# Performance work log

Hardware: AMD Instinct MI355X
Metric: run time of the kernel (lower is better)

Reference implementation:

```python
import jax, jax.numpy as jnp
import numpy as np

N_NODES = 10000
N_EDGES = 160000
LN_EPS = 1e-5
BN_EPS = 1e-5


def _leaky(x, slope=0.2):
    return jnp.where(x >= 0, x, slope * x)


def _gat_conv(x, edge_index, W, att_src, att_dst, bias, concat):
    # x: [N, Din]; W: [Din, H*C]; att_*: [H, C]
    H, C = att_src.shape
    h = (x @ W).reshape(-1, H, C)                       # [N, H, C]
    a_src = jnp.einsum('nhc,hc->nh', h, att_src)        # [N, H]
    a_dst = jnp.einsum('nhc,hc->nh', h, att_dst)
    src, dst = edge_index[0], edge_index[1]
    logits = _leaky(a_src[src] + a_dst[dst], 0.2)       # [E, H]
    # segment softmax over incoming edges of each dst node
    m = jax.ops.segment_max(logits, dst, num_segments=N_NODES)
    e = jnp.exp(logits - m[dst])
    denom = jax.ops.segment_sum(e, dst, num_segments=N_NODES)
    alpha = e / denom[dst]                              # [E, H]
    msg = h[src] * alpha[:, :, None]                    # [E, H, C]
    out = jax.ops.segment_sum(msg, dst, num_segments=N_NODES)  # [N, H, C]
    if concat:
        out = out.reshape(-1, H * C)
    else:
        out = out.mean(axis=1)
    return out + bias


def setup_inputs() -> dict:
    key = jax.random.key(0)
    ks = jax.random.split(key, 10)
    d_in, H, C = 128, 8, 64
    W = H * C  # 512
    return {
        'x': jax.random.normal(ks[0], (N_NODES, d_in), jnp.float32),
        'edge_index': jax.random.randint(ks[1], (2, N_EDGES), 0, N_NODES, jnp.int64),
        'ft_W': jax.random.normal(ks[2], (d_in, W), jnp.float32) * (1.0 / np.sqrt(d_in)),
        'ft_b': jnp.zeros((W,), jnp.float32),
        'ln_g': jnp.ones((W,), jnp.float32),
        'ln_b': jnp.zeros((W,), jnp.float32),
        'W1': jax.random.normal(ks[3], (W, H * C), jnp.float32) * (1.0 / np.sqrt(W)),
        'att_src1': jax.random.normal(ks[4], (H, C), jnp.float32) * 0.1,
        'att_dst1': jax.random.normal(ks[5], (H, C), jnp.float32) * 0.1,
        'b1': jnp.zeros((W,), jnp.float32),
        'bn_g': jnp.ones((W,), jnp.float32),
        'bn_b': jnp.zeros((W,), jnp.float32),
        'bn_mean': jnp.zeros((W,), jnp.float32),
        'bn_var': jnp.ones((W,), jnp.float32),
        'W2': jax.random.normal(ks[6], (W, H * 2), jnp.float32) * (1.0 / np.sqrt(W)),
        'att_src2': jax.random.normal(ks[7], (H, 2), jnp.float32) * 0.1,
        'att_dst2': jax.random.normal(ks[8], (H, 2), jnp.float32) * 0.1,
        'b2': jnp.zeros((2,), jnp.float32),
    }


def reference(x, edge_index, ft_W, ft_b, ln_g, ln_b, W1, att_src1, att_dst1, b1,
              bn_g, bn_b, bn_mean, bn_var, W2, att_src2, att_dst2, b2):
    # feature transform: Linear -> LayerNorm -> LeakyReLU(0.2)
    h = x @ ft_W + ft_b
    mu = h.mean(axis=-1, keepdims=True)
    var = h.var(axis=-1, keepdims=True)
    h = (h - mu) * jax.lax.rsqrt(var + LN_EPS) * ln_g + ln_b
    h = _leaky(h, 0.2)
    # GAT layer 1 (concat heads) -> BatchNorm (eval) -> ReLU  (dropout = identity in eval)
    h = _gat_conv(h, edge_index, W1, att_src1, att_dst1, b1, concat=True)
    h = (h - bn_mean) * jax.lax.rsqrt(bn_var + BN_EPS) * bn_g + bn_b
    h = jax.nn.relu(h)
    # GAT layer 2 (mean heads) -> logits [N, 2]
    logits = _gat_conv(h, edge_index, W2, att_src2, att_dst2, b2, concat=False)
    return logits
```

## Files before the change

kernel.cpp:

```cpp
#include <hip/hip_runtime.h>
#include <hip/hip_bf16.h>
#include <math.h>

#define N_NODES 10000
#define N_EDGES 160000
#define DIN 128
#define DW 512
#define NHEAD 8
#define NC 64
#define MPAD 10112
#define GEMM_BLKS 316

typedef unsigned short ushort_t;
typedef __attribute__((ext_vector_type(8))) short bf16x8;
typedef __attribute__((ext_vector_type(4))) float f32x4;

__device__ inline ushort_t f2bf(float v) {
    unsigned u = __builtin_bit_cast(unsigned, v);
    return (ushort_t)((u + 0x7fff + ((u >> 16) & 1)) >> 16);
}
__device__ inline float bf2f(ushort_t h) {
    return __builtin_bit_cast(float, (unsigned)h << 16);
}

__device__ __forceinline__ size_t swz_idx(int rb, int r, int kp, int nkt) {
    int kt = kp >> 6, kc = kp & 63;
    return ((size_t)(rb * nkt + kt)) * 8192 + r * 64 + (kc ^ ((r & 7) << 3));
}

__device__ __forceinline__ void gld16(const ushort_t* g, ushort_t* l) {
    __builtin_amdgcn_global_load_lds(
        (const __attribute__((address_space(1))) void*)g,
        (__attribute__((address_space(3))) void*)l, 16, 0, 0);
}

__global__ void k_prep(const float* __restrict__ x, const float* __restrict__ ftW,
                       const float* __restrict__ W1f,
                       ushort_t* __restrict__ Ax, ushort_t* __restrict__ Bx,
                       ushort_t* __restrict__ B1,
                       int* __restrict__ cnt, int* __restrict__ cursor) {
    int bid = blockIdx.x, t = threadIdx.x;
    if (bid < 5056) {
        int i = bid * 256 + t;
        int n = i >> 7, k = i & 127;
        float v = (n < N_NODES) ? x[n * DIN + k] : 0.f;
        ushort_t h = f2bf(v);
        ushort_t l = f2bf(v - bf2f(h));
        int rb = n >> 7, r = n & 127;
        Ax[swz_idx(rb, r, k, 4)] = h;
        Ax[swz_idx(rb, r, 128 + k, 4)] = l;
    } else if (bid < 5312) {
        int i = (bid - 5056) * 256 + t;
        int n = i >> 7, k = i & 127;
        ushort_t h = f2bf(ftW[k * DW + n]);
        int cb = n >> 7, rc = n & 127;
        Bx[swz_idx(cb, rc, k, 4)] = h;
        Bx[swz_idx(cb, rc, 128 + k, 4)] = h;
    } else if (bid < 6336) {
        int i = (bid - 5312) * 256 + t;
        int n = i >> 9, k = i & 511;
        ushort_t h = f2bf(W1f[k * DW + n]);
        int cb = n >> 7, rc = n & 127;
        B1[swz_idx(cb, rc, k, 16)] = h;
        B1[swz_idx(cb, rc, 512 + k, 16)] = h;
    } else {
        int i = (bid - 6336) * 256 + t;
        if (i < N_NODES) { cnt[i] = 0; cursor[i] = 0; }
    }
}

template<int KT, bool ATT, int EXTRA>
__global__ __launch_bounds__(256) void k_tgemm(const ushort_t* __restrict__ A,
                                               const ushort_t* __restrict__ Bm,
                                               float* __restrict__ C,
                                               ushort_t* __restrict__ Cb,
                                               const float* __restrict__ asrc,
                                               const float* __restrict__ adst,
                                               float* __restrict__ aS,
                                               float* __restrict__ aD,
                                               const int* __restrict__ ei,
                                               int* __restrict__ cnt,
                                               const int* __restrict__ off,
                                               int* __restrict__ cursor,
                                               int* __restrict__ csrc) {
    __shared__ __align__(16) ushort_t As[2][8192];
    __shared__ __align__(16) ushort_t Bs[2][8192];
    int bid = blockIdx.x;
    if (bid >= GEMM_BLKS) {
        int e = (bid - GEMM_BLKS) * 256 + threadIdx.x;
        if (e < N_EDGES) {
            if (EXTRA == 1) {
                atomicAdd(&cnt[ei[N_EDGES + e]], 1);
            } else {
                int d = ei[N_EDGES + e];
                int p = off[d] + atomicAdd(&cursor[d], 1);
                csrc[p] = ei[e];
            }
        }
        return;
    }
    int bx = bid >> 2, by = bid & 3;
    int t = threadIdx.x, w = t >> 6, l = t & 63;
    int lm = l & 15, g = l >> 4;
    int wr = w >> 1, wc = w & 1;
    int rowbase = bx * 128;
    int colbase = by * 128;

    const ushort_t* Abase = A + (size_t)bx * KT * 8192 + w * 2048 + l * 8;
    const ushort_t* Bbase = Bm + (size_t)by * KT * 8192 + w * 2048 + l * 8;

    f32x4 acc[4][4];
    #pragma unroll
    for (int r = 0; r < 4; r++)
        #pragma unroll
        for (int c = 0; c < 4; c++) acc[r][c] = (f32x4){0.f, 0.f, 0.f, 0.f};

    {
        ushort_t* la = &As[0][w * 2048];
        ushort_t* lb = &Bs[0][w * 2048];
        #pragma unroll
        for (int j = 0; j < 4; ++j) {
            gld16(Abase + j * 512, la + j * 512);
            gld16(Bbase + j * 512, lb + j * 512);
        }
    }

    int p = 0;
    for (int kt = 0; kt < KT; ++kt) {
        __builtin_amdgcn_s_barrier();
        if (kt + 1 < KT) {
            const ushort_t* ga = Abase + (size_t)(kt + 1) * 8192;
            const ushort_t* gb = Bbase + (size_t)(kt + 1) * 8192;
            ushort_t* la = &As[p ^ 1][w * 2048];
            ushort_t* lb = &Bs[p ^ 1][w * 2048];
            #pragma unroll
            for (int j = 0; j < 4; ++j) {
                gld16(ga + j * 512, la + j * 512);
                gld16(gb + j * 512, lb + j * 512);
            }
            asm volatile("s_waitcnt vmcnt(8)" ::: "memory");
        } else {
            asm volatile("s_waitcnt vmcnt(0)" ::: "memory");
        }
        __builtin_amdgcn_s_barrier();
        const char* Ap = (const char*)As[p];
        const char* Bp = (const char*)Bs[p];
        #pragma unroll
        for (int ks = 0; ks < 2; ++ks) {
            bf16x8 af[4], bfr[4];
            #pragma unroll
            for (int r = 0; r < 4; ++r) {
                int row = wr * 64 + r * 16 + lm;
                af[r] = *(const bf16x8*)(Ap + row * 128 +
                                         ((ks * 64 + g * 16) ^ ((row & 7) << 4)));
            }
            #pragma unroll
            for (int c = 0; c < 4; ++c) {
                int col = wc * 64 + c * 16 + lm;
                bfr[c] = *(const bf16x8*)(Bp + col * 128 +
                                          ((ks * 64 + g * 16) ^ ((col & 7) << 4)));
            }
            #pragma unroll
            for (int r = 0; r < 4; ++r)
                #pragma unroll
                for (int c = 0; c < 4; ++c)
                    acc[r][c] = __builtin_amdgcn_mfma_f32_16x16x32_bf16(af[r], bfr[c], acc[r][c], 0, 0, 0);
        }
        p ^= 1;
    }

    if (!ATT) {
        #pragma unroll
        for (int r = 0; r < 4; ++r) {
            int row0 = rowbase + wr * 64 + r * 16 + g * 4;
            #pragma unroll
            for (int c = 0; c < 4; ++c) {
                int col = colbase + wc * 64 + c * 16 + lm;
                #pragma unroll
                for (int q = 0; q < 4; ++q)
                    if (row0 + q < N_NODES) C[(size_t)(row0 + q) * DW + col] = acc[r][c][q];
            }
        }
    } else {
        int h = 2 * by + wc;
        float asv[4], adv[4];
        #pragma unroll
        for (int c = 0; c < 4; ++c) {
            asv[c] = asrc[h * NC + c * 16 + lm];
            adv[c] = adst[h * NC + c * 16 + lm];
        }
        #pragma unroll
        for (int r = 0; r < 4; ++r) {
            int row0 = rowbase + wr * 64 + r * 16 + g * 4;
            #pragma unroll
            for (int c = 0; c < 4; ++c) {
                int col = colbase + wc * 64 + c * 16 + lm;
                #pragma unroll
                for (int q = 0; q < 4; ++q)
                    if (row0 + q < N_NODES) Cb[(size_t)(row0 + q) * DW + col] = f2bf(acc[r][c][q]);
            }
            #pragma unroll
            for (int q = 0; q < 4; ++q) {
                float ss = acc[r][0][q] * asv[0] + acc[r][1][q] * asv[1] +
                           acc[r][2][q] * asv[2] + acc[r][3][q] * asv[3];
                float dd = acc[r][0][q] * adv[0] + acc[r][1][q] * adv[1] +
                           acc[r][2][q] * adv[2] + acc[r][3][q] * adv[3];
                #pragma unroll
                for (int m = 1; m < 16; m <<= 1) {
                    ss += __shfl_xor(ss, m, 64);
                    dd += __shfl_xor(dd, m, 64);
                }
                int row = row0 + q;
                if (lm == 0 && row < N_NODES) {
                    aS[row * NHEAD + h] = ss;
                    aD[row * NHEAD + h] = dd;
                }
            }
        }
    }
}

__global__ __launch_bounds__(256) void k_ln_scan(const float* __restrict__ hpre,
                                                 const float* __restrict__ fb,
                                                 const float* __restrict__ g,
                                                 const float* __restrict__ beta,
                                                 ushort_t* __restrict__ h0big,
                                                 const int* __restrict__ cnt,
                                                 int* __restrict__ off) {
    __shared__ int ps[256];
    __shared__ float red[8];
    int bid = blockIdx.x, t = threadIdx.x;
    if (bid == MPAD) {
        int base = t * 40;
        int loc[40];
        int s = 0;
        #pragma unroll
        for (int i = 0; i < 40; i++) {
            int idx = base + i;
            int v = idx < N_NODES ? cnt[idx] : 0;
            loc[i] = s; s += v;
        }
        ps[t] = s; __syncthreads();
        for (int o = 1; o < 256; o <<= 1) {
            int v = (t >= o) ? ps[t - o] : 0;
            __syncthreads();
            ps[t] += v;
            __syncthreads();
        }
        int pre = (t > 0) ? ps[t - 1] : 0;
        #pragma unroll
        for (int i = 0; i < 40; i++) {
            int idx = base + i;
            if (idx < N_NODES) off[idx] = pre + loc[i];
        }
        if (t == 255) off[N_NODES] = ps[255];
        return;
    }
    int n = bid;
    int rb = n >> 7, r = n & 127;
    if (n >= N_NODES) {
        #pragma unroll
        for (int j = 0; j < 4; j++)
            h0big[swz_idx(rb, r, t + j * 256, 16)] = 0;
        return;
    }
    float a0 = hpre[(size_t)n * DW + t] + fb[t];
    float a1 = hpre[(size_t)n * DW + t + 256] + fb[t + 256];
    float s = a0 + a1, sq = a0 * a0 + a1 * a1;
    for (int o = 32; o > 0; o >>= 1) { s += __shfl_down(s, o, 64); sq += __shfl_down(sq, o, 64); }
    int wid = t >> 6;
    if ((t & 63) == 0) { red[wid] = s; red[4 + wid] = sq; }
    __syncthreads();
    if (t == 0) {
        float ts = red[0] + red[1] + red[2] + red[3];
        float tq = red[4] + red[5] + red[6] + red[7];
        float mu = ts / DW;
        float var = tq / DW - mu * mu;
        red[0] = mu; red[1] = rsqrtf(var + 1e-5f);
    }
    __syncthreads();
    float mu = red[0], rs = red[1];
    float v0 = (a0 - mu) * rs * g[t] + beta[t];
    float v1 = (a1 - mu) * rs * g[t + 256] + beta[t + 256];
    v0 = v0 >= 0.f ? v0 : 0.2f * v0;
    v1 = v1 >= 0.f ? v1 : 0.2f * v1;
    ushort_t h0_ = f2bf(v0), l0_ = f2bf(v0 - bf2f(h0_));
    ushort_t h1_ = f2bf(v1), l1_ = f2bf(v1 - bf2f(h1_));
    h0big[swz_idx(rb, r, t, 16)] = h0_;
    h0big[swz_idx(rb, r, 512 + t, 16)] = l0_;
    h0big[swz_idx(rb, r, 256 + t, 16)] = h1_;
    h0big[swz_idx(rb, r, 768 + t, 16)] = l1_;
}

__global__ __launch_bounds__(256) void k_agg1csr(
    const int* __restrict__ csrc, const int* __restrict__ off,
    const ushort_t* __restrict__ h1b,
    const float* __restrict__ aS, const float* __restrict__ aD,
    const float* __restrict__ b1, const float* __restrict__ bnm,
    const float* __restrict__ bnv, const float* __restrict__ bng,
    const float* __restrict__ bnb, ushort_t* __restrict__ h2b)
{
    int n = blockIdx.x, t = threadIdx.x;
    int beg = off[n], end = off[n + 1];
    __shared__ float wls[64][NHEAD];
    __shared__ int   sls[64];
    __shared__ float aDn[NHEAD];
    __shared__ float dsum[NHEAD];
    if (t < NHEAD) { aDn[t] = aD[n * NHEAD + t]; dsum[t] = 0.f; }
    __syncthreads();
    float acc0 = 0.f, acc1 = 0.f, dpart = 0.f;
    int hA = t >> 5;
    for (int c = beg; c < end; c += 64) {
        int m = min(64, end - c);
        if (t < m) sls[t] = csrc[c + t];
        __syncthreads();
        for (int idx = t; idx < m * NHEAD; idx += 256) {
            int el = idx >> 3, h = idx & 7;
            float l = aS[sls[el] * NHEAD + h] + aDn[h];
            l = l >= 0.f ? l : 0.2f * l;
            float w = __expf(l);
            wls[el][h] = w;
            dpart += w;
        }
        __syncthreads();
        for (int el = 0; el < m; el++) {
            float w = wls[el][hA];
            unsigned v = *(const unsigned*)(h1b + (size_t)sls[el] * DW + 2 * t);
            acc0 += w * __builtin_bit_cast(float, v << 16);
            acc1 += w * __builtin_bit_cast(float, v & 0xffff0000u);
        }
        __syncthreads();
    }
    for (int o = 8; o < 64; o <<= 1) dpart += __shfl_down(dpart, o, 64);
    if ((t & 63) < NHEAD) atomicAdd(&dsum[t & 7], dpart);
    __syncthreads();
    float rd = dsum[hA] > 0.f ? 1.f / dsum[hA] : 0.f;
    int j0 = 2 * t, j1 = 2 * t + 1;
    float v0 = acc0 * rd + b1[j0];
    v0 = (v0 - bnm[j0]) * rsqrtf(bnv[j0] + 1e-5f) * bng[j0] + bnb[j0];
    v0 = v0 > 0.f ? v0 : 0.f;
    float v1 = acc1 * rd + b1[j1];
    v1 = (v1 - bnm[j1]) * rsqrtf(bnv[j1] + 1e-5f) * bng[j1] + bnb[j1];
    v1 = v1 > 0.f ? v1 : 0.f;
    unsigned pk = (unsigned)f2bf(v0) | ((unsigned)f2bf(v1) << 16);
    *(unsigned*)(h2b + (size_t)n * DW + 2 * t) = pk;
}

__global__ __launch_bounds__(256) void k_gemm2att(const ushort_t* __restrict__ h2b,
                                                  const float* __restrict__ W2,
                                                  const float* __restrict__ as2,
                                                  const float* __restrict__ ad2,
                                                  float* __restrict__ gout,
                                                  float* __restrict__ aS,
                                                  float* __restrict__ aD) {
    __shared__ float Ws[DW * 16];
    __shared__ float gl[16][16];
    __shared__ float a2[32];
    int t = threadIdx.x;
    for (int i = t; i < DW * 16; i += 256) Ws[i] = W2[i];
    if (t < 16) a2[t] = as2[t];
    else if (t < 32) a2[t] = ad2[t - 16];
    __syncthreads();
    int nb = blockIdx.x * 16;
    int nl = t >> 4, j = t & 15;
    const bf16x8* hr = (const bf16x8*)(h2b + (size_t)(nb + nl) * DW);
    float acc = 0.f;
    for (int ks = 0; ks < DW / 8; ks++) {
        bf16x8 v = hr[ks];
        #pragma unroll
        for (int u = 0; u < 8; u++)
            acc += bf2f((ushort_t)v[u]) * Ws[(ks * 8 + u) * 16 + j];
    }
    gout[(nb + nl) * 16 + j] = acc;
    gl[nl][j] = acc;
    __syncthreads();
    if (j < 8) {
        aS[(nb + nl) * NHEAD + j] = gl[nl][2 * j] * a2[2 * j] + gl[nl][2 * j + 1] * a2[2 * j + 1];
    } else {
        int h = j - 8;
        aD[(nb + nl) * NHEAD + h] = gl[nl][2 * h] * a2[16 + 2 * h] + gl[nl][2 * h + 1] * a2[16 + 2 * h + 1];
    }
}

__global__ __launch_bounds__(256) void k_agg2csr(
    const int* __restrict__ csrc, const int* __restrict__ off,
    const float* __restrict__ gbuf,
    const float* __restrict__ aS, const float* __restrict__ aD,
    const float* __restrict__ b2, float* __restrict__ outp)
{
    int t = threadIdx.x;
    int n = blockIdx.x * 4 + (t >> 6);
    int lane = t & 63;
    if (n >= N_NODES) return;
    int beg = off[n], end = off[n + 1];
    int j = lane & 15, slot = lane >> 4, h = j >> 1;
    float adn = aD[n * NHEAD + h];
    float acc = 0.f, den = 0.f;
    for (int c = beg + slot; c < end; c += 4) {
        int s = csrc[c];
        float l = aS[s * NHEAD + h] + adn;
        l = l >= 0.f ? l : 0.2f * l;
        float w = __expf(l);
        den += w;
        acc += w * gbuf[s * 16 + j];
    }
    acc += __shfl_down(acc, 16, 64); acc += __shfl_down(acc, 32, 64);
    den += __shfl_down(den, 16, 64); den += __shfl_down(den, 32, 64);
    float v = (lane < 16 && den > 0.f) ? acc / den : 0.f;
    v += __shfl_down(v, 2, 64);
    v += __shfl_down(v, 4, 64);
    v += __shfl_down(v, 8, 64);
    if (lane < 2) outp[n * 2 + lane] = v * 0.125f + b2[lane];
}

extern "C" void kernel_launch(void* const* d_in, const int* in_sizes, int n_in,
                              void* d_out, int out_size, void* d_ws, size_t ws_size,
                              hipStream_t stream) {
    const float* x    = (const float*)d_in[0];
    const int*   ei   = (const int*)d_in[1];
    const float* ftW  = (const float*)d_in[2];
    const float* ftb  = (const float*)d_in[3];
    const float* lng  = (const float*)d_in[4];
    const float* lnb  = (const float*)d_in[5];
    const float* W1   = (const float*)d_in[6];
    const float* as1  = (const float*)d_in[7];
    const float* ad1  = (const float*)d_in[8];
    const float* b1   = (const float*)d_in[9];
    const float* bng  = (const float*)d_in[10];
    const float* bnb  = (const float*)d_in[11];
    const float* bnm  = (const float*)d_in[12];
    const float* bnv  = (const float*)d_in[13];
    const float* W2   = (const float*)d_in[14];
    const float* as2  = (const float*)d_in[15];
    const float* ad2  = (const float*)d_in[16];
    const float* b2   = (const float*)d_in[17];
    float* out = (float*)d_out;

    float* F = (float*)d_ws;
    ushort_t* Ax    = (ushort_t*)(F + 0);
    float*    gbuf  = F + 0;
    ushort_t* Bx    = (ushort_t*)(F + 1294336);
    ushort_t* B1    = (ushort_t*)(F + 1359872);
    float*    hpre  = F + 1622016;
    ushort_t* h2b   = (ushort_t*)(F + 1622016);
    ushort_t* h0big = (ushort_t*)(F + 6799360);
    ushort_t* h1b   = (ushort_t*)(F + 11976704);
    float*    aS1   = F + 14536704;
    float*    aD1   = F + 14616704;
    int* cnt        = (int*)(F + 14696704);
    int* cursor     = (int*)(F + 14706704);
    int* off        = (int*)(F + 14716704);
    int* csrc       = (int*)(F + 14726705);

    k_prep<<<6376, 256, 0, stream>>>(x, ftW, W1, Ax, Bx, B1, cnt, cursor);
    k_tgemm<4, false, 1><<<GEMM_BLKS + 625, 256, 0, stream>>>(
        Ax, Bx, hpre, nullptr, nullptr, nullptr, nullptr, nullptr,
        ei, cnt, nullptr, nullptr, nullptr);
    k_ln_scan<<<MPAD + 1, 256, 0, stream>>>(hpre, ftb, lng, lnb, h0big, cnt, off);
    k_tgemm<16, true, 2><<<GEMM_BLKS + 625, 256, 0, stream>>>(
        h0big, B1, nullptr, h1b, as1, ad1, aS1, aD1,
        ei, nullptr, off, cursor, csrc);
    k_agg1csr<<<N_NODES, 256, 0, stream>>>(csrc, off, h1b, aS1, aD1, b1, bnm, bnv, bng, bnb, h2b);
    k_gemm2att<<<N_NODES / 16, 256, 0, stream>>>(h2b, W2, as2, ad2, gbuf, aS1, aD1);
    k_agg2csr<<<(N_NODES + 3) / 4, 256, 0, stream>>>(csrc, off, gbuf, aS1, aD1, b2, out);
}
```

Baseline: 131.0 us.

## Use 512-thread GEMM blocks and vectorize swizzled bf16 stores in prep and LayerNorm

The tiled bf16 MFMA GEMM now runs 8 waves per 128x128 tile instead of 4. Each wave computes a 32x64 sub-tile, so accumulator registers are halved and `__launch_bounds__(512,4)` asks for more resident waves. The tile loads are redistributed across 512 threads, and the edge-count/CSR-fill tail blocks now cover 512 edges each. The input hi/lo split in k_prep and the LayerNorm output writes in k_ln_scan now use 16-byte vector stores into the swizzled layout; the LayerNorm path stages through shared memory with an extra barrier. The aim is better latency hiding in the GEMMs and fewer scattered 2-byte stores, at the cost of more LDS reads of B fragments per tile and extra sync.

```diff
diff --git a/kernel.cpp b/kernel.cpp
--- a/kernel.cpp
+++ b/kernel.cpp
@@ -13,6 +13,7 @@
 
 typedef unsigned short ushort_t;
 typedef __attribute__((ext_vector_type(8))) short bf16x8;
+typedef __attribute__((ext_vector_type(8))) unsigned short us8;
 typedef __attribute__((ext_vector_type(4))) float f32x4;
 
 __device__ inline ushort_t f2bf(float v) {
@@ -40,54 +41,66 @@
                        ushort_t* __restrict__ B1,
                        int* __restrict__ cnt, int* __restrict__ cursor) {
     int bid = blockIdx.x, t = threadIdx.x;
-    if (bid < 5056) {
-        int i = bid * 256 + t;
-        int n = i >> 7, k = i & 127;
-        float v = (n < N_NODES) ? x[n * DIN + k] : 0.f;
-        ushort_t h = f2bf(v);
-        ushort_t l = f2bf(v - bf2f(h));
+    if (bid < 632) {
+        int gid = bid * 256 + t;
+        int n = gid >> 4, k0 = (gid & 15) * 8;
+        float v[8];
+        if (n < N_NODES) {
+            #pragma unroll
+            for (int u = 0; u < 8; u++) v[u] = x[n * DIN + k0 + u];
+        } else {
+            #pragma unroll
+            for (int u = 0; u < 8; u++) v[u] = 0.f;
+        }
+        us8 hi, lo;
+        #pragma unroll
+        for (int u = 0; u < 8; u++) {
+            ushort_t h = f2bf(v[u]);
+            hi[u] = h;
+            lo[u] = f2bf(v[u] - bf2f(h));
+        }
         int rb = n >> 7, r = n & 127;
-        Ax[swz_idx(rb, r, k, 4)] = h;
-        Ax[swz_idx(rb, r, 128 + k, 4)] = l;
-    } else if (bid < 5312) {
-        int i = (bid - 5056) * 256 + t;
+        *(us8*)(Ax + swz_idx(rb, r, k0, 4)) = hi;
+        *(us8*)(Ax + swz_idx(rb, r, 128 + k0, 4)) = lo;
+    } else if (bid < 888) {
+        int i = (bid - 632) * 256 + t;
         int n = i >> 7, k = i & 127;
         ushort_t h = f2bf(ftW[k * DW + n]);
         int cb = n >> 7, rc = n & 127;
         Bx[swz_idx(cb, rc, k, 4)] = h;
         Bx[swz_idx(cb, rc, 128 + k, 4)] = h;
-    } else if (bid < 6336) {
-        int i = (bid - 5312) * 256 + t;
+    } else if (bid < 1912) {
+        int i = (bid - 888) * 256 + t;
         int n = i >> 9, k = i & 511;
         ushort_t h = f2bf(W1f[k * DW + n]);
         int cb = n >> 7, rc = n & 127;
         B1[swz_idx(cb, rc, k, 16)] = h;
         B1[swz_idx(cb, rc, 512 + k, 16)] = h;
     } else {
-        int i = (bid - 6336) * 256 + t;
+        int i = (bid - 1912) * 256 + t;
         if (i < N_NODES) { cnt[i] = 0; cursor[i] = 0; }
     }
 }
 
 template<int KT, bool ATT, int EXTRA>
-__global__ __launch_bounds__(256) void k_tgemm(const ushort_t* __restrict__ A,
-                                               const ushort_t* __restrict__ Bm,
-                                               float* __restrict__ C,
-                                               ushort_t* __restrict__ Cb,
-                                               const float* __restrict__ asrc,
-                                               const float* __restrict__ adst,
-                                               float* __restrict__ aS,
-                                               float* __restrict__ aD,
-                                               const int* __restrict__ ei,
-                                               int* __restrict__ cnt,
-                                               const int* __restrict__ off,
-                                               int* __restrict__ cursor,
-                                               int* __restrict__ csrc) {
+__global__ __launch_bounds__(512, 4) void k_tgemm(const ushort_t* __restrict__ A,
+                                                  const ushort_t* __restrict__ Bm,
+                                                  float* __restrict__ C,
+                                                  ushort_t* __restrict__ Cb,
+                                                  const float* __restrict__ asrc,
+                                                  const float* __restrict__ adst,
+                                                  float* __restrict__ aS,
+                                                  float* __restrict__ aD,
+                                                  const int* __restrict__ ei,
+                                                  int* __restrict__ cnt,
+                                                  const int* __restrict__ off,
+                                                  int* __restrict__ cursor,
+                                                  int* __restrict__ csrc) {
     __shared__ __align__(16) ushort_t As[2][8192];
     __shared__ __align__(16) ushort_t Bs[2][8192];
     int bid = blockIdx.x;
     if (bid >= GEMM_BLKS) {
-        int e = (bid - GEMM_BLKS) * 256 + threadIdx.x;
+        int e = (bid - GEMM_BLKS) * 512 + threadIdx.x;
         if (e < N_EDGES) {
             if (EXTRA == 1) {
                 atomicAdd(&cnt[ei[N_EDGES + e]], 1);
@@ -106,22 +119,20 @@
     int rowbase = bx * 128;
     int colbase = by * 128;
 
-    const ushort_t* Abase = A + (size_t)bx * KT * 8192 + w * 2048 + l * 8;
-    const ushort_t* Bbase = Bm + (size_t)by * KT * 8192 + w * 2048 + l * 8;
-
-    f32x4 acc[4][4];
+    const ushort_t* Abase = A + (size_t)bx * KT * 8192 + t * 8;
+    const ushort_t* Bbase = Bm + (size_t)by * KT * 8192 + t * 8;
+
+    f32x4 acc[2][4];
     #pragma unroll
-    for (int r = 0; r < 4; r++)
+    for (int r = 0; r < 2; r++)
         #pragma unroll
         for (int c = 0; c < 4; c++) acc[r][c] = (f32x4){0.f, 0.f, 0.f, 0.f};
 
     {
-        ushort_t* la = &As[0][w * 2048];
-        ushort_t* lb = &Bs[0][w * 2048];
-        #pragma unroll
-        for (int j = 0; j < 4; ++j) {
-            gld16(Abase + j * 512, la + j * 512);
-            gld16(Bbase + j * 512, lb + j * 512);
+        #pragma unroll
+        for (int j = 0; j < 2; ++j) {
+            gld16(Abase + j * 4096, &As[0][j * 4096 + t * 8]);
+            gld16(Bbase + j * 4096, &Bs[0][j * 4096 + t * 8]);
         }
     }
 
@@ -131,14 +142,12 @@
         if (kt + 1 < KT) {
             const ushort_t* ga = Abase + (size_t)(kt + 1) * 8192;
             const ushort_t* gb = Bbase + (size_t)(kt + 1) * 8192;
-            ushort_t* la = &As[p ^ 1][w * 2048];
-            ushort_t* lb = &Bs[p ^ 1][w * 2048];
-            #pragma unroll
-            for (int j = 0; j < 4; ++j) {
-                gld16(ga + j * 512, la + j * 512);
-                gld16(gb + j * 512, lb + j * 512);
-            }
-            asm volatile("s_waitcnt vmcnt(8)" ::: "memory");
+            #pragma unroll
+            for (int j = 0; j < 2; ++j) {
+                gld16(ga + j * 4096, &As[p ^ 1][j * 4096 + t * 8]);
+                gld16(gb + j * 4096, &Bs[p ^ 1][j * 4096 + t * 8]);
+            }
+            asm volatile("s_waitcnt vmcnt(4)" ::: "memory");
         } else {
             asm volatile("s_waitcnt vmcnt(0)" ::: "memory");
         }
@@ -147,10 +156,10 @@
         const char* Bp = (const char*)Bs[p];
         #pragma unroll
         for (int ks = 0; ks < 2; ++ks) {
-            bf16x8 af[4], bfr[4];
-            #pragma unroll
-            for (int r = 0; r < 4; ++r) {
-                int row = wr * 64 + r * 16 + lm;
+            bf16x8 af[2], bfr[4];
+            #pragma unroll
+            for (int r = 0; r < 2; ++r) {
+                int row = wr * 32 + r * 16 + lm;
                 af[r] = *(const bf16x8*)(Ap + row * 128 +
                                          ((ks * 64 + g * 16) ^ ((row & 7) << 4)));
             }
@@ -161,7 +170,7 @@
                                           ((ks * 64 + g * 16) ^ ((col & 7) << 4)));
             }
             #pragma unroll
-            for (int r = 0; r < 4; ++r)
+            for (int r = 0; r < 2; ++r)
                 #pragma unroll
                 for (int c = 0; c < 4; ++c)
                     acc[r][c] = __builtin_amdgcn_mfma_f32_16x16x32_bf16(af[r], bfr[c], acc[r][c], 0, 0, 0);
@@ -171,8 +180,8 @@
 
     if (!ATT) {
         #pragma unroll
-        for (int r = 0; r < 4; ++r) {
-            int row0 = rowbase + wr * 64 + r * 16 + g * 4;
+        for (int r = 0; r < 2; ++r) {
+            int row0 = rowbase + wr * 32 + r * 16 + g * 4;
             #pragma unroll
             for (int c = 0; c < 4; ++c) {
                 int col = colbase + wc * 64 + c * 16 + lm;
@@ -190,8 +199,8 @@
             adv[c] = adst[h * NC + c * 16 + lm];
         }
         #pragma unroll
-        for (int r = 0; r < 4; ++r) {
-            int row0 = rowbase + wr * 64 + r * 16 + g * 4;
+        for (int r = 0; r < 2; ++r) {
+            int row0 = rowbase + wr * 32 + r * 16 + g * 4;
             #pragma unroll
             for (int c = 0; c < 4; ++c) {
                 int col = colbase + wc * 64 + c * 16 + lm;
@@ -229,6 +238,7 @@
                                                  int* __restrict__ off) {
     __shared__ int ps[256];
     __shared__ float red[8];
+    __shared__ __align__(16) ushort_t st[1024];
     int bid = blockIdx.x, t = threadIdx.x;
     if (bid == MPAD) {
         int base = t * 40;
@@ -259,9 +269,11 @@
     int n = bid;
     int rb = n >> 7, r = n & 127;
     if (n >= N_NODES) {
-        #pragma unroll
-        for (int j = 0; j < 4; j++)
-            h0big[swz_idx(rb, r, t + j * 256, 16)] = 0;
+        if (t < 128) {
+            int kp0 = t * 8;
+            *(us8*)(h0big + ((size_t)(rb * 16 + (kp0 >> 6))) * 8192 + r * 64 +
+                    ((kp0 & 63) ^ ((r & 7) << 3))) = (us8){0,0,0,0,0,0,0,0};
+        }
         return;
     }
     float a0 = hpre[(size_t)n * DW + t] + fb[t];
@@ -286,10 +298,14 @@
     v1 = v1 >= 0.f ? v1 : 0.2f * v1;
     ushort_t h0_ = f2bf(v0), l0_ = f2bf(v0 - bf2f(h0_));
     ushort_t h1_ = f2bf(v1), l1_ = f2bf(v1 - bf2f(h1_));
-    h0big[swz_idx(rb, r, t, 16)] = h0_;
-    h0big[swz_idx(rb, r, 512 + t, 16)] = l0_;
-    h0big[swz_idx(rb, r, 256 + t, 16)] = h1_;
-    h0big[swz_idx(rb, r, 768 + t, 16)] = l1_;
+    st[t] = h0_;        st[256 + t] = h1_;
+    st[512 + t] = l0_;  st[768 + t] = l1_;
+    __syncthreads();
+    if (t < 128) {
+        int kp0 = t * 8;
+        *(us8*)(h0big + ((size_t)(rb * 16 + (kp0 >> 6))) * 8192 + r * 64 +
+                ((kp0 & 63) ^ ((r & 7) << 3))) = *(const us8*)(st + kp0);
+    }
 }
 
 __global__ __launch_bounds__(256) void k_agg1csr(
@@ -452,12 +468,12 @@
     int* off        = (int*)(F + 14716704);
     int* csrc       = (int*)(F + 14726705);
 
-    k_prep<<<6376, 256, 0, stream>>>(x, ftW, W1, Ax, Bx, B1, cnt, cursor);
-    k_tgemm<4, false, 1><<<GEMM_BLKS + 625, 256, 0, stream>>>(
+    k_prep<<<1952, 256, 0, stream>>>(x, ftW, W1, Ax, Bx, B1, cnt, cursor);
+    k_tgemm<4, false, 1><<<GEMM_BLKS + 313, 512, 0, stream>>>(
         Ax, Bx, hpre, nullptr, nullptr, nullptr, nullptr, nullptr,
         ei, cnt, nullptr, nullptr, nullptr);
     k_ln_scan<<<MPAD + 1, 256, 0, stream>>>(hpre, ftb, lng, lnb, h0big, cnt, off);
-    k_tgemm<16, true, 2><<<GEMM_BLKS + 625, 256, 0, stream>>>(
+    k_tgemm<16, true, 2><<<GEMM_BLKS + 313, 512, 0, stream>>>(
         h0big, B1, nullptr, h1b, as1, ad1, aS1, aD1,
         ei, nullptr, off, cursor, csrc);
     k_agg1csr<<<N_NODES, 256, 0, stream>>>(csrc, off, h1b, aS1, aD1, b1, bnm, bnv, bng, bnb, h2b);
```

Measured after the change: 126.1 us. 1.04x faster.
